# Optimization experiments

Hardware: AMD Instinct MI355X
Metric: run time of the kernel (lower is better)

Reference implementation:

```python
import jax, jax.numpy as jnp
import numpy as np

R = 100        # voxel grid resolution per axis
N = 200000     # number of active (non-empty) voxels
K = 3          # kernel size
CIN = 64
COUT = 64
NOFF = K ** 3 - 1  # 26 non-center offsets


def _build_maps():
    # Mirrors mapping_cuda: per kernel offset, find (input_row, output_row) pairs
    # such that coords[input] == coords[output] + offset (submanifold conv,
    # output coords == input coords).
    rng = np.random.default_rng(0)
    lin = rng.choice(R ** 3, size=N, replace=False)
    coords = np.stack(np.unravel_index(lin, (R, R, R)), axis=1)  # [N,3]
    lut = np.full(R ** 3, -1, dtype=np.int64)
    lut[lin] = np.arange(N)
    offs = [(dx, dy, dz) for dx in (-1, 0, 1) for dy in (-1, 0, 1)
            for dz in (-1, 0, 1) if (dx, dy, dz) != (0, 0, 0)]
    ins, outs = [], []
    for d in offs:
        tgt = coords - np.asarray(d)              # output coord receiving input i
        valid = np.all((tgt >= 0) & (tgt < R), axis=1)
        idx_i = np.nonzero(valid)[0]
        tlin = np.ravel_multi_index(tgt[valid].T, (R, R, R))
        j = lut[tlin]
        hit = j >= 0
        ins.append(idx_i[hit].astype(np.int32))
        outs.append(j[hit].astype(np.int32))
    P = max(len(a) for a in ins)
    imap = np.full((NOFF, P), -1, dtype=np.int32)
    omap = np.full((NOFF, P), -1, dtype=np.int32)
    for k, (a, b) in enumerate(zip(ins, outs)):
        imap[k, :len(a)] = a
        omap[k, :len(b)] = b
    return jnp.asarray(imap), jnp.asarray(omap)


def setup_inputs() -> dict:
    key = jax.random.key(0)
    kf, kw = jax.random.split(key)
    feats = jax.random.normal(kf, (N, CIN), dtype=jnp.float32)
    # reset_parameters: uniform(-stdv, stdv), stdv = 1/sqrt(out_channels * K^3)
    stdv = 1.0 / float(np.sqrt(COUT * K ** 3))
    kernel = jax.random.uniform(kw, (K ** 3, CIN, COUT), dtype=jnp.float32,
                                minval=-stdv, maxval=stdv)
    imap, omap = _build_maps()
    return {"feats": feats, "kernel": kernel, "imap": imap, "omap": omap}


def reference(feats, kernel, imap, omap):
    # Submanifold sparse 3D conv: gather -> per-offset GEMM -> scatter-add.
    K3 = kernel.shape[0]
    c = K3 // 2  # center offset: identity neighbor map
    w_nc = jnp.concatenate([kernel[:c], kernel[c + 1:]], axis=0)  # [26,Cin,Cout]
    mask = imap >= 0                                   # [26,P]
    gath = feats[jnp.where(mask, imap, 0)] * mask[..., None]   # [26,P,Cin]
    y = jnp.einsum('kpc,kco->kpo', gath, w_nc)         # [26,P,Cout]
    out = feats @ kernel[c]                            # center contribution [N,Cout]
    oi = jnp.where(mask, omap, 0).reshape(-1)          # masked rows add zeros at row 0
    out = out.at[oi].add(y.reshape(-1, y.shape[-1]))
    return out
```

## Files before the change

kernel.cpp:

```cpp
#include <hip/hip_runtime.h>


#define CIN 64
#define COUT 64
#define TR 32
#define NOFF 26

typedef short bf16x8 __attribute__((ext_vector_type(8)));
typedef unsigned short ushort8 __attribute__((ext_vector_type(8)));
typedef float f32x4 __attribute__((ext_vector_type(4)));

__device__ inline unsigned short bfbits(float f) {
    unsigned u = __builtin_bit_cast(unsigned, f);
    u += 0x7fffu + ((u >> 16) & 1u);
    return (unsigned short)(u >> 16);
}

__device__ inline constexpr int kk_of_item(int i) {
    return (i >= 26) ? 13 : 26 - (i < 13 ? i : i + 1);
}

__global__ __launch_bounds__(256) void prep_all(
    const float* __restrict__ feats, unsigned short* __restrict__ fb,
    const float* __restrict__ W, unsigned short* __restrict__ Wt,
    const int* __restrict__ imap, int* __restrict__ rg,
    int N, int P, int nt, int FB)
{
    const int bid = blockIdx.x, tid = threadIdx.x;
    if (bid < FB) {
        const int i8 = (bid * 256 + tid) * 8;
        const int nf = N * 64;
        if (i8 >= (N + 1) * 64) return;
        union { unsigned short u[8]; bf16x8 v; } r;
        if (i8 >= nf) {
            r.v = (bf16x8)0;
        } else {
            const float4 v0 = *(const float4*)(feats + i8);
            const float4 v1 = *(const float4*)(feats + i8 + 4);
            r.u[0] = bfbits(v0.x); r.u[1] = bfbits(v0.y);
            r.u[2] = bfbits(v0.z); r.u[3] = bfbits(v0.w);
            r.u[4] = bfbits(v1.x); r.u[5] = bfbits(v1.y);
            r.u[6] = bfbits(v1.z); r.u[7] = bfbits(v1.w);
        }
        *(bf16x8*)(fb + i8) = r.v;
    } else if (bid < FB + 27) {
        const int k = bid - FB;
        for (int idx = tid; idx < CIN * COUT; idx += 256) {
            const int c = idx >> 6, o = idx & 63;
            const int q = c >> 3, e = c & 7;
            Wt[((k * 64 + o) * 64) + (((q ^ (o & 7)) << 3) + e)] =
                bfbits(W[(k * 64 + c) * 64 + o]);
        }
    } else {
        const int idx = (bid - FB - 27) * 256 + tid;
        const int nt1 = nt + 1;
        if (idx >= NOFF * nt1) return;
        const int m = idx / nt1, tile = idx % nt1;
        const int* a = imap + (size_t)m * P;
        const int target = tile * TR;
        int lo = 0, hi = P;
        while (lo < hi) {
            const int mid = (lo + hi) >> 1;
            const int v = a[mid];
            const int key = (v < 0) ? 0x7fffffff : v;
            if (key < target) lo = mid + 1; else hi = mid;
        }
        rg[(size_t)m * nt1 + tile] = lo;
    }
}

__global__ __launch_bounds__(256, 4) void spconv_v10(
    const unsigned short* __restrict__ fb,
    const unsigned short* __restrict__ wt,
    const int* __restrict__ imap, const int* __restrict__ omap,
    const int* __restrict__ rg,
    float* __restrict__ out, int N, int P, int nt, int nwg)
{
    __shared__ unsigned short wbuf[2][4096];
    __shared__ int srctab[4][3][32];

    const int tid = threadIdx.x, w = tid >> 6, lane = tid & 63;
    const int col = lane & 15, grp = lane >> 4;

    const int orig = blockIdx.x;
    const int q = nwg >> 3, r8 = nwg & 7;
    const int xcd = orig & 7, kb = orig >> 3;
    const int sb = (xcd < r8 ? xcd * (q + 1) : r8 * (q + 1) + (xcd - r8) * q) + kb;

    const int t = sb * 4 + w;
    const int tt = (t < nt) ? t : (nt - 1);
    const int r0 = t * TR;
    const int nt1 = nt + 1;

    int p0a[27], cnta[27];
    int mva[27];
    bf16x8 af[27][2][2];
    ushort8 wr[27][2];

    auto RGLOAD = [&](int j) {
        const int* rp = rg + (size_t)j * nt1 + tt;
        p0a[j] = rp[0];
        cnta[j] = rp[1];
    };
    auto MAPS = [&](int j) {
        const int p0 = p0a[j];
        const int cnt = cnta[j] - p0;
        cnta[j] = cnt;
        int idx = p0 + ((lane < cnt) ? lane : 0);
        idx = (idx < P) ? idx : P - 1;
        const int iv = imap[(size_t)j * P + idx];
        const int ov = omap[(size_t)j * P + idx];
        mva[j] = (ov << 6) | ((iv - r0) & 63);
    };
    auto STWRITE = [&](int j) {
        int* st = srctab[w][j % 3];
        if (lane < 32) st[lane] = N;
        if (lane < cnta[j]) st[mva[j] & 63] = mva[j] >> 6;
    };
    auto READGATHER = [&](int j) {
        int s0, s1;
        if (j < 26) {
            const int* st = srctab[w][j % 3];
            s0 = st[col];
            s1 = st[col + 16];
        } else {
            const int ra = r0 + col, rb = r0 + 16 + col;
            s0 = (ra < N) ? ra : N;
            s1 = (rb < N) ? rb : N;
        }
        const bf16x8* fp = (const bf16x8*)(fb + (size_t)s0 * 64 + grp * 8);
        af[j][0][0] = fp[0];
        af[j][0][1] = fp[4];
        const bf16x8* fq = (const bf16x8*)(fb + (size_t)s1 * 64 + grp * 8);
        af[j][1][0] = fq[0];
        af[j][1][1] = fq[4];
    };

#pragma unroll
    for (int j = 0; j < 4; ++j) if (j < 26) RGLOAD(j);
#pragma unroll
    for (int j = 0; j < 3; ++j) if (j < 26) MAPS(j);
    STWRITE(0); STWRITE(1);

    {
        const unsigned short* wk0 = wt + kk_of_item(0) * 4096;
        const ushort8 t0 = *(const ushort8*)(wk0 + tid * 8);
        const ushort8 t1 = *(const ushort8*)(wk0 + 2048 + tid * 8);
        const unsigned short* wk1 = wt + kk_of_item(1) * 4096;
        wr[1][0] = *(const ushort8*)(wk1 + tid * 8);
        wr[1][1] = *(const ushort8*)(wk1 + 2048 + tid * 8);
        *(ushort8*)(&wbuf[0][tid * 8]) = t0;
        *(ushort8*)(&wbuf[0][2048 + tid * 8]) = t1;
    }
    READGATHER(0);
    asm volatile("s_waitcnt lgkmcnt(0)" ::: "memory");
    __builtin_amdgcn_s_barrier();

    f32x4 acc[2][4];
#pragma unroll
    for (int s = 0; s < 2; ++s)
#pragma unroll
        for (int ot = 0; ot < 4; ++ot) acc[s][ot] = {0.f, 0.f, 0.f, 0.f};

#pragma unroll
    for (int it = 0; it < 27; ++it) {
        if (it + 4 < 26) RGLOAD(it + 4);
        if (it + 3 < 26) MAPS(it + 3);
        if (it + 2 < 26) STWRITE(it + 2);
        if (it + 1 <= 26) READGATHER(it + 1);
        if (it + 2 <= 26) {
            const unsigned short* wk = wt + kk_of_item(it + 2) * 4096;
            wr[it + 2][0] = *(const ushort8*)(wk + tid * 8);
            wr[it + 2][1] = *(const ushort8*)(wk + 2048 + tid * 8);
        }
        if (it + 1 <= 26) {
            unsigned short* nb = wbuf[(it + 1) & 1];
            *(ushort8*)(&nb[tid * 8]) = wr[it + 1][0];
            *(ushort8*)(&nb[2048 + tid * 8]) = wr[it + 1][1];
        }
        const unsigned short* cb = wbuf[it & 1];
        __builtin_amdgcn_s_setprio(1);
#pragma unroll
        for (int ot = 0; ot < 4; ++ot) {
            const int o = ot * 16 + col;
            const bf16x8 b0 = *(const bf16x8*)(cb + o * 64 + ((grp ^ (col & 7)) << 3));
            const bf16x8 b1 = *(const bf16x8*)(cb + o * 64 + (((4 + grp) ^ (col & 7)) << 3));
#pragma unroll
            for (int s = 0; s < 2; ++s) {
                acc[s][ot] = __builtin_amdgcn_mfma_f32_16x16x32_bf16(af[it][s][0], b0, acc[s][ot], 0, 0, 0);
                acc[s][ot] = __builtin_amdgcn_mfma_f32_16x16x32_bf16(af[it][s][1], b1, acc[s][ot], 0, 0, 0);
            }
        }
        __builtin_amdgcn_s_setprio(0);
        if (it < 26) {
            asm volatile("s_waitcnt lgkmcnt(0)" ::: "memory");
            __builtin_amdgcn_s_barrier();
        }
    }

#pragma unroll
    for (int s = 0; s < 2; ++s)
#pragma unroll
        for (int ot = 0; ot < 4; ++ot) {
            const f32x4 cv = acc[s][ot];
#pragma unroll
            for (int reg = 0; reg < 4; ++reg) {
                const int rr = r0 + s * 16 + grp * 4 + reg;
                if (rr < N) out[(size_t)rr * 64 + ot * 16 + col] = cv[reg];
            }
        }
}

template <int MODE>
__global__ __launch_bounds__(256) void spconv_fb(
    const float* __restrict__ feats, const float* __restrict__ W,
    const int* __restrict__ imap, const int* __restrict__ omap,
    float* __restrict__ out, int npairs)
{
    __shared__ float4 wt4[16 * 64];
    const int tid = threadIdx.x, koff = blockIdx.y;
    const float* Wk;
    const int* im = nullptr; const int* om = nullptr;
    if (MODE == 0) Wk = W + 13 * (CIN * COUT);
    else {
        const int kk = (koff < 13) ? koff : koff + 1;
        Wk = W + (size_t)kk * (CIN * COUT);
        im = imap + (size_t)koff * npairs; om = omap + (size_t)koff * npairs;
    }
    float* wts = (float*)wt4;
    for (int idx = tid; idx < CIN * COUT; idx += 256) {
        const int c = idx >> 6, o = idx & 63;
        wts[((c >> 2) * 64 + o) * 4 + (c & 3)] = Wk[idx];
    }
    __syncthreads();
    const int o = tid & 63, w = tid >> 6;
    const int base = blockIdx.x * 256 + w * 64;
    const float4* f4p = (const float4*)feats;
    for (int n = 0; n < 64; ++n) {
        const int p = base + n;
        if (p >= npairs) break;
        int i, j;
        if (MODE == 0) { i = p; j = p; }
        else { i = im[p]; if (i < 0) continue; j = om[p]; }
        i = __builtin_amdgcn_readfirstlane(i);
        float a = 0.f;
#pragma unroll
        for (int c4 = 0; c4 < 16; ++c4) {
            const float4 f = f4p[(size_t)i * 16 + c4];
            const float4 wv = wt4[c4 * 64 + o];
            a += f.x * wv.x + f.y * wv.y + f.z * wv.z + f.w * wv.w;
        }
        if (MODE == 0) out[(size_t)j * COUT + o] = a;
        else atomicAdd(&out[(size_t)j * COUT + o], a);
    }
}

extern "C" void kernel_launch(void* const* d_in, const int* in_sizes, int n_in,
                              void* d_out, int out_size, void* d_ws, size_t ws_size,
                              hipStream_t stream) {
    const float* feats = (const float*)d_in[0];
    const float* W     = (const float*)d_in[1];
    const int* imap    = (const int*)d_in[2];
    const int* omap    = (const int*)d_in[3];
    float* out         = (float*)d_out;

    const int N = in_sizes[0] / CIN;
    const int P = in_sizes[2] / NOFF;
    const int nt = (N + TR - 1) / TR;
    const int nt1 = nt + 1;

    const size_t fb_bytes = (size_t)(N + 1) * 64 * sizeof(unsigned short);
    const size_t wt_bytes = 27 * 64 * 64 * sizeof(unsigned short);
    const size_t rg_bytes = (size_t)NOFF * nt1 * sizeof(int);

    if (ws_size < fb_bytes + wt_bytes + rg_bytes) {
        dim3 blk(256);
        dim3 gc((N + 255) / 256, 1);
        spconv_fb<0><<<gc, blk, 0, stream>>>(feats, W, nullptr, nullptr, out, N);
        dim3 go((P + 255) / 256, NOFF);
        spconv_fb<1><<<go, blk, 0, stream>>>(feats, W, imap, omap, out, P);
        return;
    }

    unsigned short* fbp = (unsigned short*)d_ws;
    unsigned short* Wt  = (unsigned short*)((char*)d_ws + fb_bytes);
    int* rg             = (int*)((char*)d_ws + fb_bytes + wt_bytes);

    const int FB  = ((N + 1) * 64 + 2047) / 2048;
    const int RGB = (NOFF * nt1 + 255) / 256;
    prep_all<<<FB + 27 + RGB, 256, 0, stream>>>(feats, fbp, W, Wt, imap, rg,
                                                N, P, nt, FB);

    const int nwg = (nt + 3) / 4;
    spconv_v10<<<nwg, 256, 0, stream>>>(fbp, Wt, imap, omap, rg, out,
                                        N, P, nt, nwg);
}
```

Before: 88.21 us.

## Load weights directly as MFMA fragments from global, drop LDS staging and barriers

The prep kernel now writes the bf16 weights pre-arranged in MFMA B-fragment order, so each lane reads its eight 16-byte fragments for the current offset straight from global (L2-resident) memory. The double-buffered LDS weight staging and the per-iteration s_waitcnt plus workgroup barrier are removed, so the four waves are no longer forced into lockstep. In exchange each wave loads the full 8 KB weight slice itself, four times the global/L2 traffic of before, and those loads are issued in the same iteration that consumes them, exposing their latency.

```diff
diff --git a/kernel.cpp b/kernel.cpp
--- a/kernel.cpp
+++ b/kernel.cpp
@@ -7,7 +7,6 @@
 #define NOFF 26
 
 typedef short bf16x8 __attribute__((ext_vector_type(8)));
-typedef unsigned short ushort8 __attribute__((ext_vector_type(8)));
 typedef float f32x4 __attribute__((ext_vector_type(4)));
 
 __device__ inline unsigned short bfbits(float f) {
@@ -22,7 +21,7 @@
 
 __global__ __launch_bounds__(256) void prep_all(
     const float* __restrict__ feats, unsigned short* __restrict__ fb,
-    const float* __restrict__ W, unsigned short* __restrict__ Wt,
+    const float* __restrict__ W, unsigned short* __restrict__ wf,
     const int* __restrict__ imap, int* __restrict__ rg,
     int N, int P, int nt, int FB)
 {
@@ -46,10 +45,10 @@
     } else if (bid < FB + 27) {
         const int k = bid - FB;
         for (int idx = tid; idx < CIN * COUT; idx += 256) {
-            const int c = idx >> 6, o = idx & 63;
-            const int q = c >> 3, e = c & 7;
-            Wt[((k * 64 + o) * 64) + (((q ^ (o & 7)) << 3) + e)] =
-                bfbits(W[(k * 64 + c) * 64 + o]);
+            const int j = idx >> 9, l = (idx >> 3) & 63, e = idx & 7;
+            const int o = (j >> 1) * 16 + (l & 15);
+            const int c = (j & 1) * 32 + (l >> 4) * 8 + e;
+            wf[k * 4096 + idx] = bfbits(W[(k * 64 + c) * 64 + o]);
         }
     } else {
         const int idx = (bid - FB - 27) * 256 + tid;
@@ -69,14 +68,13 @@
     }
 }
 
-__global__ __launch_bounds__(256, 4) void spconv_v10(
+__global__ __launch_bounds__(256, 4) void spconv_v11(
     const unsigned short* __restrict__ fb,
-    const unsigned short* __restrict__ wt,
+    const unsigned short* __restrict__ wf,
     const int* __restrict__ imap, const int* __restrict__ omap,
     const int* __restrict__ rg,
     float* __restrict__ out, int N, int P, int nt, int nwg)
 {
-    __shared__ unsigned short wbuf[2][4096];
     __shared__ int srctab[4][3][32];
 
     const int tid = threadIdx.x, w = tid >> 6, lane = tid & 63;
@@ -95,7 +93,6 @@
     int p0a[27], cnta[27];
     int mva[27];
     bf16x8 af[27][2][2];
-    ushort8 wr[27][2];
 
     auto RGLOAD = [&](int j) {
         const int* rp = rg + (size_t)j * nt1 + tt;
@@ -137,24 +134,11 @@
     };
 
 #pragma unroll
-    for (int j = 0; j < 4; ++j) if (j < 26) RGLOAD(j);
-#pragma unroll
-    for (int j = 0; j < 3; ++j) if (j < 26) MAPS(j);
+    for (int j = 0; j < 4; ++j) RGLOAD(j);
+#pragma unroll
+    for (int j = 0; j < 3; ++j) MAPS(j);
     STWRITE(0); STWRITE(1);
-
-    {
-        const unsigned short* wk0 = wt + kk_of_item(0) * 4096;
-        const ushort8 t0 = *(const ushort8*)(wk0 + tid * 8);
-        const ushort8 t1 = *(const ushort8*)(wk0 + 2048 + tid * 8);
-        const unsigned short* wk1 = wt + kk_of_item(1) * 4096;
-        wr[1][0] = *(const ushort8*)(wk1 + tid * 8);
-        wr[1][1] = *(const ushort8*)(wk1 + 2048 + tid * 8);
-        *(ushort8*)(&wbuf[0][tid * 8]) = t0;
-        *(ushort8*)(&wbuf[0][2048 + tid * 8]) = t1;
-    }
     READGATHER(0);
-    asm volatile("s_waitcnt lgkmcnt(0)" ::: "memory");
-    __builtin_amdgcn_s_barrier();
 
     f32x4 acc[2][4];
 #pragma unroll
@@ -167,35 +151,27 @@
         if (it + 4 < 26) RGLOAD(it + 4);
         if (it + 3 < 26) MAPS(it + 3);
         if (it + 2 < 26) STWRITE(it + 2);
+
+        bf16x8 frw[8];
+        {
+            const unsigned short* wk = wf + kk_of_item(it) * 4096;
+#pragma unroll
+            for (int j = 0; j < 8; ++j)
+                frw[j] = *(const bf16x8*)(wk + j * 512 + lane * 8);
+        }
+
         if (it + 1 <= 26) READGATHER(it + 1);
-        if (it + 2 <= 26) {
-            const unsigned short* wk = wt + kk_of_item(it + 2) * 4096;
-            wr[it + 2][0] = *(const ushort8*)(wk + tid * 8);
-            wr[it + 2][1] = *(const ushort8*)(wk + 2048 + tid * 8);
-        }
-        if (it + 1 <= 26) {
-            unsigned short* nb = wbuf[(it + 1) & 1];
-            *(ushort8*)(&nb[tid * 8]) = wr[it + 1][0];
-            *(ushort8*)(&nb[2048 + tid * 8]) = wr[it + 1][1];
-        }
-        const unsigned short* cb = wbuf[it & 1];
+
         __builtin_amdgcn_s_setprio(1);
 #pragma unroll
         for (int ot = 0; ot < 4; ++ot) {
-            const int o = ot * 16 + col;
-            const bf16x8 b0 = *(const bf16x8*)(cb + o * 64 + ((grp ^ (col & 7)) << 3));
-            const bf16x8 b1 = *(const bf16x8*)(cb + o * 64 + (((4 + grp) ^ (col & 7)) << 3));
 #pragma unroll
             for (int s = 0; s < 2; ++s) {
-                acc[s][ot] = __builtin_amdgcn_mfma_f32_16x16x32_bf16(af[it][s][0], b0, acc[s][ot], 0, 0, 0);
-                acc[s][ot] = __builtin_amdgcn_mfma_f32_16x16x32_bf16(af[it][s][1], b1, acc[s][ot], 0, 0, 0);
+                acc[s][ot] = __builtin_amdgcn_mfma_f32_16x16x32_bf16(af[it][s][0], frw[ot * 2 + 0], acc[s][ot], 0, 0, 0);
+                acc[s][ot] = __builtin_amdgcn_mfma_f32_16x16x32_bf16(af[it][s][1], frw[ot * 2 + 1], acc[s][ot], 0, 0, 0);
             }
         }
         __builtin_amdgcn_s_setprio(0);
-        if (it < 26) {
-            asm volatile("s_waitcnt lgkmcnt(0)" ::: "memory");
-            __builtin_amdgcn_s_barrier();
-        }
     }
 
 #pragma unroll
@@ -270,10 +246,10 @@
     const int nt1 = nt + 1;
 
     const size_t fb_bytes = (size_t)(N + 1) * 64 * sizeof(unsigned short);
-    const size_t wt_bytes = 27 * 64 * 64 * sizeof(unsigned short);
+    const size_t wf_bytes = 27 * 64 * 64 * sizeof(unsigned short);
     const size_t rg_bytes = (size_t)NOFF * nt1 * sizeof(int);
 
-    if (ws_size < fb_bytes + wt_bytes + rg_bytes) {
+    if (ws_size < fb_bytes + wf_bytes + rg_bytes) {
         dim3 blk(256);
         dim3 gc((N + 255) / 256, 1);
         spconv_fb<0><<<gc, blk, 0, stream>>>(feats, W, nullptr, nullptr, out, N);
@@ -283,15 +259,15 @@
     }
 
     unsigned short* fbp = (unsigned short*)d_ws;
-    unsigned short* Wt  = (unsigned short*)((char*)d_ws + fb_bytes);
-    int* rg             = (int*)((char*)d_ws + fb_bytes + wt_bytes);
+    unsigned short* wf  = (unsigned short*)((char*)d_ws + fb_bytes);
+    int* rg             = (int*)((char*)d_ws + fb_bytes + wf_bytes);
 
     const int FB  = ((N + 1) * 64 + 2047) / 2048;
     const int RGB = (NOFF * nt1 + 255) / 256;
-    prep_all<<<FB + 27 + RGB, 256, 0, stream>>>(feats, fbp, W, Wt, imap, rg,
+    prep_all<<<FB + 27 + RGB, 256, 0, stream>>>(feats, fbp, W, wf, imap, rg,
                                                 N, P, nt, FB);
 
     const int nwg = (nt + 3) / 4;
-    spconv_v10<<<nwg, 256, 0, stream>>>(fbp, Wt, imap, omap, rg, out,
+    spconv_v11<<<nwg, 256, 0, stream>>>(fbp, wf, imap, omap, rg, out,
                                         N, P, nt, nwg);
 }
```

Measured after the change: 117.0 us. +32.7%, slower.
